# Optimization experiments

Hardware: AMD Instinct MI355X
Metric: run time of the kernel (lower is better)

## Reference

```python
import jax, jax.numpy as jnp
import numpy as np

EMBED_DIM = 128
NUM_HEADS = 16
D_K = EMBED_DIM // NUM_HEADS  # 8 quantum wires


def setup_inputs() -> dict:
    key = jax.random.key(0)
    k_x, k_theta, k_w = jax.random.split(key, 3)
    x = jax.random.normal(k_x, (2, 2048, EMBED_DIM), dtype=jnp.float32)
    # trainable RX angles, one per wire (shared across q/k/v since the same
    # q_layer is applied three times in the original module)
    theta = jax.random.normal(k_theta, (D_K,), dtype=jnp.float32)
    # combine_heads Linear(embed_dim, embed_dim, bias=False): weight [out, in]
    bound = 1.0 / np.sqrt(EMBED_DIM)
    W_combine = jax.random.uniform(k_w, (EMBED_DIM, EMBED_DIM), dtype=jnp.float32,
                                   minval=-bound, maxval=bound)
    return {"x": x, "theta": theta, "W_combine": W_combine}


def reference(x, theta, W_combine):
    B, S, E = x.shape
    H, dk = NUM_HEADS, D_K
    # Quantum circuit closed form: RX(x_i) encode then RX(theta_i), no
    # entanglement -> <PauliZ_i> = cos(x_i + theta_i), per token per head.
    z = jnp.cos(x.reshape(B, S, H, dk) + theta)          # [B,S,H,dk]
    # q = k = v = z (same _apply_q applied to x three times)
    qh = z.transpose(0, 2, 1, 3)                          # [B,H,S,dk]
    scores = jnp.einsum("bhsd,bhtd->bhst", qh, qh) / jnp.sqrt(jnp.float32(dk))
    attn = jax.nn.softmax(scores, axis=-1)                # [B,H,S,S]
    out = jnp.einsum("bhst,bhtd->bhsd", attn, qh)         # [B,H,S,dk]
    out = out.transpose(0, 2, 1, 3).reshape(B, S, E)      # [B,S,E]
    return out @ W_combine.T
```

## Files before the change

kernel.cpp:

```cpp
#include <hip/hip_runtime.h>

#define SEQ   2048
#define EMB   128
#define NH    16
#define NB    2
#define NBH   (NB * NH)
#define QB    128
#define NQB   (SEQ / QB)
#define SEQ_H 1024
#define K1_THREADS 512

typedef _Float16 half_t;
typedef _Float16 half4  __attribute__((ext_vector_type(4)));
typedef __fp16   fp16x2 __attribute__((ext_vector_type(2)));
typedef float    floatx16 __attribute__((ext_vector_type(16)));

#define SMEM_BYTES 36944
#define ZT_OFF     16384
#define ZT_PITCH   2056

__global__ __launch_bounds__(K1_THREADS, 8)
void qattn_mfma_kernel(const float* __restrict__ x,
                       const float* __restrict__ theta,
                       half_t* __restrict__ pD,
                       float* __restrict__ lbuf)
{
    __shared__ __align__(16) char smem[SMEM_BYTES];

    const int tid = threadIdx.x;
    const int bid = blockIdx.x;
    const int c2  = bid & 1;
    const int qb  = (bid >> 1) & (NQB - 1);
    const int bh  = bid >> 5;
    const int b   = bh >> 4;
    const int h   = bh & (NH - 1);

    float th[8];
#pragma unroll
    for (int d = 0; d < 8; ++d) th[d] = theta[d];

    const float4* x4 = (const float4*)x + (size_t)b * SEQ * (EMB / 4) + h * 2;

    half4* zqk0 = (half4*)smem;
    half4* zqk1 = (half4*)(smem + 8192);

#pragma unroll
    for (int i = 0; i < SEQ_H / K1_THREADS; ++i) {
        const int tl = tid + i * K1_THREADS;
        const int tg = c2 * SEQ_H + tl;
        float4 lo  = x4[(size_t)tg * (EMB / 4)];
        float4 hi4 = x4[(size_t)tg * (EMB / 4) + 1];
        float z0 = __cosf(lo.x  + th[0]);
        float z1 = __cosf(lo.y  + th[1]);
        float z2 = __cosf(lo.z  + th[2]);
        float z3 = __cosf(lo.w  + th[3]);
        float z4 = __cosf(hi4.x + th[4]);
        float z5 = __cosf(hi4.y + th[5]);
        float z6 = __cosf(hi4.z + th[6]);
        float z7 = __cosf(hi4.w + th[7]);
        half4 zl, zh;
        zl[0] = (half_t)z0; zl[1] = (half_t)z1; zl[2] = (half_t)z2; zl[3] = (half_t)z3;
        zh[0] = (half_t)z4; zh[1] = (half_t)z5; zh[2] = (half_t)z6; zh[3] = (half_t)z7;
        zqk0[tl] = zl;
        zqk1[tl] = zh;
#pragma unroll
        for (int d = 0; d < 4; ++d)
            *(half_t*)(smem + ZT_OFF + d * ZT_PITCH + tl * 2) = zl[d];
#pragma unroll
        for (int d = 0; d < 4; ++d)
            *(half_t*)(smem + ZT_OFF + (4 + d) * ZT_PITCH + tl * 2) = zh[d];
        *(half_t*)(smem + ZT_OFF + 8 * ZT_PITCH + tl * 2) = (half_t)1.0f;
        *(half_t*)(smem + ZT_OFF + 9 * ZT_PITCH + tl * 2) = (half_t)0.0f;
    }

    const int lane = tid & 63;
    const int wid  = tid >> 6;
    const int g    = wid & 3;
    const int c    = wid >> 2;
    const int ln   = lane & 31;
    const int hi   = lane >> 5;

    const float C = 0.35355339059327373f * 1.4426950408889634f;
    const int q = qb * QB + g * 32 + ln;
    float4 xq = ((const float4*)x)[(size_t)(b * SEQ + q) * (EMB / 4) + h * 2 + hi];
    half4 qf;
    qf[0] = (half_t)(__cosf(xq.x + th[4 * hi + 0]) * C);
    qf[1] = (half_t)(__cosf(xq.y + th[4 * hi + 1]) * C);
    qf[2] = (half_t)(__cosf(xq.z + th[4 * hi + 2]) * C);
    qf[3] = (half_t)(__cosf(xq.w + th[4 * hi + 3]) * C);

    __syncthreads();

    const half4* kp  = (hi ? zqk1 : zqk0) + ln;
    const int    dcl = (ln < 9) ? ln : 9;
    const half4* vp  = (const half4*)(smem + ZT_OFF + dcl * ZT_PITCH + hi * 8);

    floatx16 acc = {};
    const floatx16 zero16 = {};
    const int tb = c * (SEQ_H / 2);

#pragma unroll 4
    for (int tt = 0; tt < SEQ_H / 2; tt += 32) {
        const int t0 = tb + tt;
        half4 kf = kp[t0];
        floatx16 s = __builtin_amdgcn_mfma_f32_32x32x8f16(kf, qf, zero16, 0, 0, 0);
        float p[16];
#pragma unroll
        for (int r = 0; r < 16; ++r) p[r] = __builtin_amdgcn_exp2f(s[r]);
#pragma unroll
        for (int w = 0; w < 4; ++w) {
            union { half4 h4; fp16x2 f2[2]; } u;
            u.f2[0] = __builtin_amdgcn_cvt_pkrtz(p[4 * w + 0], p[4 * w + 1]);
            u.f2[1] = __builtin_amdgcn_cvt_pkrtz(p[4 * w + 2], p[4 * w + 3]);
            half4 vf = vp[(t0 >> 2) + 2 * w];
            acc = __builtin_amdgcn_mfma_f32_32x32x8f16(u.h4, vf, acc, 0, 0, 0);
        }
    }

    __syncthreads();
    float* red = (float*)smem;
    const int slot = (g * 64 + lane) * 17;
    if (c == 1) {
#pragma unroll
        for (int r = 0; r < 16; ++r) red[slot + r] = acc[r];
    }
    __syncthreads();
    if (c == 0) {
#pragma unroll
        for (int r = 0; r < 16; ++r) acc[r] += red[slot + r];

        const int q0 = qb * QB + g * 32 + 4 * hi;
        if (ln < 8) {
#pragma unroll
            for (int r = 0; r < 16; ++r) {
                const int qq = q0 + (r & 3) + 8 * (r >> 2);
                pD[((size_t)(b * SEQ + qq) * 2 + c2) * EMB + h * 8 + ln] = (half_t)acc[r];
            }
        } else if (ln == 8) {
#pragma unroll
            for (int r = 0; r < 16; ++r) {
                const int qq = q0 + (r & 3) + 8 * (r >> 2);
                lbuf[(size_t)(b * SEQ + qq) * 32 + c2 * 16 + h] = acc[r];
            }
        }
    }
}

#define K2_ROWS 16
#define K2_THREADS 512
#define WT_STRIDE 132

__global__ __launch_bounds__(K2_THREADS) void combine_kernel(const half_t* pD,
                                                             const float* __restrict__ lbuf,
                                                             const float* __restrict__ W,
                                                             float* out) {
    __shared__ float Wt[128 * WT_STRIDE];
    __shared__ float Xs[K2_ROWS * 128];

    const int tid   = threadIdx.x;
    const int rbase = blockIdx.x * K2_ROWS;

    for (int i = tid; i < 128 * 128; i += K2_THREADS) {
        int e = i >> 7, k = i & 127;
        Wt[k * WT_STRIDE + e] = W[i];
    }
#pragma unroll
    for (int j = 0; j < (K2_ROWS * 128) / K2_THREADS; ++j) {
        const int i = tid + j * K2_THREADS;
        const int r = i >> 7, k = i & 127, hh = k >> 3;
        const int row = rbase + r;
        float p = (float)pD[(size_t)row * 256 + k] + (float)pD[(size_t)row * 256 + 128 + k];
        float l = lbuf[(size_t)row * 32 + hh] + lbuf[(size_t)row * 32 + 16 + hh];
        Xs[i] = p * __builtin_amdgcn_rcpf(l);
    }
    __syncthreads();

    const int r = tid >> 5;
    const int g = tid & 31;
    float4 acc = make_float4(0.f, 0.f, 0.f, 0.f);

    const float4* X4 = (const float4*)&Xs[r * 128];
#pragma unroll
    for (int kc = 0; kc < 32; ++kc) {
        float4 x4 = X4[kc];
#pragma unroll
        for (int j = 0; j < 4; ++j) {
            int k = kc * 4 + j;
            float4 w = *(const float4*)&Wt[k * WT_STRIDE + g * 4];
            float xv = (j == 0) ? x4.x : (j == 1) ? x4.y : (j == 2) ? x4.z : x4.w;
            acc.x = fmaf(xv, w.x, acc.x);
            acc.y = fmaf(xv, w.y, acc.y);
            acc.z = fmaf(xv, w.z, acc.z);
            acc.w = fmaf(xv, w.w, acc.w);
        }
    }

    ((float4*)out)[(size_t)(rbase + r) * 32 + g] = acc;
}

extern "C" void kernel_launch(void* const* d_in, const int* in_sizes, int n_in,
                              void* d_out, int out_size, void* d_ws, size_t ws_size,
                              hipStream_t stream) {
    const float* x     = (const float*)d_in[0];
    const float* theta = (const float*)d_in[1];
    const float* W     = (const float*)d_in[2];
    float*  out  = (float*)d_out;
    half_t* pD   = (half_t*)d_out;
    float*  lbuf = (float*)d_ws;

    qattn_mfma_kernel<<<NBH * NQB * 2, K1_THREADS, 0, stream>>>(x, theta, pD, lbuf);
    combine_kernel<<<(NB * SEQ) / K2_ROWS, K2_THREADS, 0, stream>>>(pD, lbuf, W, out);
}
```

Baseline: 30.13 us.

## Rewrite combine projection as fp16 MFMA GEMM with larger row tiles

Replaces the scalar fp32 FMA combine kernel with one that converts W and the normalized attention output to fp16 in shared memory and computes the 32x128 output tile per block with 32x32x8 MFMA instructions. Rows per block double to 32, so the W staging and transpose cost is paid over twice as many rows and there are half as many blocks. W is loaded with coalesced float4 reads and no longer transposed. This lowers the precision of the final projection to fp16 inputs with fp32 accumulation.

```diff
diff --git a/kernel.cpp b/kernel.cpp
--- a/kernel.cpp
+++ b/kernel.cpp
@@ -146,56 +146,68 @@
     }
 }
 
-#define K2_ROWS 16
-#define K2_THREADS 512
-#define WT_STRIDE 132
-
-__global__ __launch_bounds__(K2_THREADS) void combine_kernel(const half_t* pD,
-                                                             const float* __restrict__ lbuf,
-                                                             const float* __restrict__ W,
-                                                             float* out) {
-    __shared__ float Wt[128 * WT_STRIDE];
-    __shared__ float Xs[K2_ROWS * 128];
+#define K2_ROWS    32
+#define K2_THREADS 256
+#define XW_PITCH   132
+
+__global__ __launch_bounds__(K2_THREADS)
+void combine_mfma_kernel(const half_t* pD,
+                         const float* __restrict__ lbuf,
+                         const float* __restrict__ W,
+                         float* out)
+{
+    __shared__ half_t Ws[128 * XW_PITCH];
+    __shared__ half_t Xs[K2_ROWS * XW_PITCH];
 
     const int tid   = threadIdx.x;
     const int rbase = blockIdx.x * K2_ROWS;
 
-    for (int i = tid; i < 128 * 128; i += K2_THREADS) {
-        int e = i >> 7, k = i & 127;
-        Wt[k * WT_STRIDE + e] = W[i];
-    }
-#pragma unroll
-    for (int j = 0; j < (K2_ROWS * 128) / K2_THREADS; ++j) {
-        const int i = tid + j * K2_THREADS;
-        const int r = i >> 7, k = i & 127, hh = k >> 3;
+#pragma unroll
+    for (int it = 0; it < 16; ++it) {
+        const int idx = tid + it * K2_THREADS;
+        const int e   = idx >> 5;
+        const int k4  = idx & 31;
+        float4 w = ((const float4*)W)[idx];
+        union { half4 h4; fp16x2 f2[2]; } u;
+        u.f2[0] = __builtin_amdgcn_cvt_pkrtz(w.x, w.y);
+        u.f2[1] = __builtin_amdgcn_cvt_pkrtz(w.z, w.w);
+        *(half4*)&Ws[e * XW_PITCH + 4 * k4] = u.h4;
+    }
+#pragma unroll
+    for (int it = 0; it < 8; ++it) {
+        const int idx = tid + it * K2_THREADS;
+        const int r   = idx >> 6;
+        const int k2  = idx & 63;
         const int row = rbase + r;
-        float p = (float)pD[(size_t)row * 256 + k] + (float)pD[(size_t)row * 256 + 128 + k];
-        float l = lbuf[(size_t)row * 32 + hh] + lbuf[(size_t)row * 32 + 16 + hh];
-        Xs[i] = p * __builtin_amdgcn_rcpf(l);
-    }
-    __syncthreads();
-
-    const int r = tid >> 5;
-    const int g = tid & 31;
-    float4 acc = make_float4(0.f, 0.f, 0.f, 0.f);
-
-    const float4* X4 = (const float4*)&Xs[r * 128];
-#pragma unroll
-    for (int kc = 0; kc < 32; ++kc) {
-        float4 x4 = X4[kc];
-#pragma unroll
-        for (int j = 0; j < 4; ++j) {
-            int k = kc * 4 + j;
-            float4 w = *(const float4*)&Wt[k * WT_STRIDE + g * 4];
-            float xv = (j == 0) ? x4.x : (j == 1) ? x4.y : (j == 2) ? x4.z : x4.w;
-            acc.x = fmaf(xv, w.x, acc.x);
-            acc.y = fmaf(xv, w.y, acc.y);
-            acc.z = fmaf(xv, w.z, acc.z);
-            acc.w = fmaf(xv, w.w, acc.w);
-        }
-    }
-
-    ((float4*)out)[(size_t)(rbase + r) * 32 + g] = acc;
+        const half_t* p0 = &pD[(size_t)row * 256 + 2 * k2];
+        const int hh = k2 >> 2;
+        float l  = lbuf[(size_t)row * 32 + hh] + lbuf[(size_t)row * 32 + 16 + hh];
+        float rl = __builtin_amdgcn_rcpf(l);
+        float v0 = ((float)p0[0] + (float)p0[128]) * rl;
+        float v1 = ((float)p0[1] + (float)p0[129]) * rl;
+        *(fp16x2*)&Xs[r * XW_PITCH + 2 * k2] = __builtin_amdgcn_cvt_pkrtz(v0, v1);
+    }
+    __syncthreads();
+
+    const int lane = tid & 63;
+    const int wv   = tid >> 6;
+    const int ln   = lane & 31;
+    const int hi   = lane >> 5;
+    const int e0   = wv * 32;
+
+    floatx16 acc = {};
+#pragma unroll
+    for (int kk = 0; kk < 16; ++kk) {
+        half4 a = *(const half4*)&Xs[ln * XW_PITCH + kk * 8 + hi * 4];
+        half4 bf = *(const half4*)&Ws[(e0 + ln) * XW_PITCH + kk * 8 + hi * 4];
+        acc = __builtin_amdgcn_mfma_f32_32x32x8f16(a, bf, acc, 0, 0, 0);
+    }
+
+#pragma unroll
+    for (int reg = 0; reg < 16; ++reg) {
+        const int r_loc = (reg & 3) + 8 * (reg >> 2) + 4 * hi;
+        out[(size_t)(rbase + r_loc) * EMB + e0 + ln] = acc[reg];
+    }
 }
 
 extern "C" void kernel_launch(void* const* d_in, const int* in_sizes, int n_in,
@@ -209,5 +221,5 @@
     float*  lbuf = (float*)d_ws;
 
     qattn_mfma_kernel<<<NBH * NQB * 2, K1_THREADS, 0, stream>>>(x, theta, pD, lbuf);
-    combine_kernel<<<(NB * SEQ) / K2_ROWS, K2_THREADS, 0, stream>>>(pD, lbuf, W, out);
+    combine_mfma_kernel<<<(NB * SEQ) / K2_ROWS, K2_THREADS, 0, stream>>>(pD, lbuf, W, out);
 }
```

Result: faster. 28.07 us (-6.8%).
